# Performance work log

Hardware: AMD Instinct MI355X
Metric: run time of the kernel (lower is better)

## Reference

```python
import jax, jax.numpy as jnp
import numpy as np

NTOKENS = 8192
TOPK = 2
E = 8
K = 1024  # hidden
N = 1024  # ffn shard (ffn_hidden // ffn_tp)


def setup_inputs() -> dict:
    key = jax.random.key(0)
    k1, k2, k3 = jax.random.split(key, 3)
    x = jax.random.normal(k1, (NTOKENS, K), jnp.float32) * 0.02
    # weights stored [E, N, K] (transpose_weight=True path in the torch module)
    weights = jax.random.normal(k2, (E, N, K), jnp.float32) * 0.02
    # random top-k expert assignment per token, then derive the expert-sorted
    # dispatch permutation (scatter_index) and per-expert counts (splits),
    # exactly the invariants flux.prepare_moe_ag_scatter_args relies on.
    experts = jax.random.randint(k3, (NTOKENS, TOPK), 0, E)
    flat = experts.reshape(-1)                       # [NTOKENS*TOPK]
    order = jnp.argsort(flat, stable=True)           # output row -> flat slot
    m = NTOKENS * TOPK
    pos = jnp.zeros((m,), jnp.int32).at[order].set(jnp.arange(m, dtype=jnp.int32))
    scatter_index = pos.reshape(NTOKENS, TOPK)       # flat slot -> output row
    splits = jnp.bincount(flat, length=E).astype(jnp.int32)
    return {"x": x, "weights": weights, "scatter_index": scatter_index, "splits": splits}


def reference(x, weights, scatter_index, splits):
    """MoE AG-scatter grouped GEMM (single-rank semantics: all-gather = identity).

    For each output row s (rows sorted by expert): out[s] = x[token(s)] @ W[e(s)].T
    where token(s) = gather_A_index[s] // topk and e(s) comes from splits.
    """
    ntokens, topk = scatter_index.shape
    e, n, k = weights.shape
    m_out = ntokens * topk  # total dispatched rows
    # inverse permutation: output row s -> flattened (token, slot) index
    gather_a = jnp.argsort(scatter_index.reshape(-1), stable=True)  # [m_out]
    token_of_row = gather_a // topk                                  # [m_out]
    expert_of_row = jnp.repeat(jnp.arange(e, dtype=jnp.int32), splits,
                               total_repeat_length=m_out)            # [m_out]
    # compute each token against every expert once (E/topk redundancy), then
    # gather the (token, expert) pairs -- avoids per-row weight materialization
    y_all = jnp.einsum('tk,enk->ten', x, weights)   # [ntokens, E, N]
    out = y_all[token_of_row, expert_of_row]        # [m_out, N]
    return out
```

## Files before the change

### kernel.cpp

```cpp
#include <hip/hip_runtime.h>
#include <hip/hip_bf16.h>

#define NTOK   8192
#define TOPK   2
#define NEXP   8
#define KDIM   1024
#define NDIM   1024
#define MOUT   (NTOK * TOPK)
#define BM     128
#define BN     128
#define BK     64
#define MAXT   (MOUT / BM + NEXP)
#define ROWTOK 1024

#define XB_OFF   (128 * 1024)
#define XB_BYTES (NTOK * KDIM * 2)
#define WB_OFF   (XB_OFF + XB_BYTES)
#define WB_BYTES (NEXP * NDIM * KDIM * 2)
#define WS_NEED  ((size_t)(WB_OFF + WB_BYTES))

typedef unsigned short ushort_t;
typedef __attribute__((ext_vector_type(8))) short short8;
typedef __attribute__((ext_vector_type(4))) float floatx4;
typedef __attribute__((address_space(1))) const unsigned int gu32;
typedef __attribute__((address_space(3))) unsigned int lu32;

__global__ void moe_setup(const int* __restrict__ scatter,
                          const int* __restrict__ splits,
                          int* __restrict__ ws) {
  int tid = blockIdx.x * blockDim.x + threadIdx.x;
  if (tid < MOUT) {
    int s = scatter[tid];
    ws[ROWTOK + s] = tid / TOPK;
  }
  if (tid == 0) {
    int nt = 0, off = 0;
    for (int e = 0; e < NEXP; ++e) {
      int end = off + splits[e];
      for (int r0 = off; r0 < end; r0 += BM) {
        ws[16 + 3 * nt + 0] = r0;
        ws[16 + 3 * nt + 1] = (end - r0 < BM) ? (end - r0) : BM;
        ws[16 + 3 * nt + 2] = e;
        ++nt;
      }
      off = end;
    }
    ws[0] = nt;
    for (int t = nt; t < MAXT; ++t) {
      ws[16 + 3 * t + 0] = 0;
      ws[16 + 3 * t + 1] = 0;
      ws[16 + 3 * t + 2] = 0;
    }
  }
}

__global__ __launch_bounds__(256)
void convert_both(const float* __restrict__ x, const float* __restrict__ w,
                  ushort_t* __restrict__ xb, ushort_t* __restrict__ wb) {
  const int N4X = NTOK * KDIM / 4;
  const int N4W = NEXP * NDIM * KDIM / 4;
  int idx = blockIdx.x * 256 + threadIdx.x;
  for (int i = idx; i < N4X + N4W; i += gridDim.x * 256) {
    float4 v = (i < N4X) ? ((const float4*)x)[i] : ((const float4*)w)[i - N4X];
    union { __hip_bfloat162 h; unsigned int u; } lo, hi;
    lo.h = __float22bfloat162_rn(make_float2(v.x, v.y));
    hi.h = __float22bfloat162_rn(make_float2(v.z, v.w));
    uint2 u2; u2.x = lo.u; u2.y = hi.u;
    if (i < N4X) ((uint2*)xb)[i] = u2;
    else         ((uint2*)wb)[i - N4X] = u2;
  }
}

__global__ __launch_bounds__(256, 3)
void moe_gemm_fast(const ushort_t* __restrict__ xb,
                   const ushort_t* __restrict__ wbm,
                   const int* __restrict__ ws,
                   float* __restrict__ out) {
  __shared__ ushort_t As[BM * BK];
  __shared__ ushort_t Bs[BN * BK];

  const int slot = blockIdx.x;
  const int rows = ws[16 + 3 * slot + 1];
  if (rows == 0) return;
  const int row0 = ws[16 + 3 * slot + 0];
  const int e    = ws[16 + 3 * slot + 2];
  const int c0   = blockIdx.y * BN;

  const int tid  = threadIdx.x;
  const int lane = tid & 63;
  const int wave = tid >> 6;
  const int wm   = (wave >> 1) * 64;
  const int wn   = (wave & 1) * 64;
  const int quad = lane >> 4;
  const int l16  = lane & 15;

  const int* __restrict__ row_token = ws + ROWTOK;

  const int lrow8  = lane >> 3;
  const int gchunk = (lane & 7) ^ lrow8;

  const ushort_t* aptr[4];
  const ushort_t* bptr[4];
#pragma unroll
  for (int t = 0; t < 4; ++t) {
    int r  = wave * 32 + t * 8 + lrow8;
    int rc = (r < rows) ? r : (rows - 1);
    aptr[t] = xb + (size_t)row_token[row0 + rc] * KDIM + gchunk * 8;
    bptr[t] = wbm + ((size_t)e * NDIM + c0 + r) * KDIM + gchunk * 8;
  }

  floatx4 zero = {0.f, 0.f, 0.f, 0.f};
  floatx4 acc[4][4];
#pragma unroll
  for (int i = 0; i < 4; ++i)
#pragma unroll
    for (int j = 0; j < 4; ++j) acc[i][j] = zero;

#pragma unroll 4
  for (int kk = 0; kk < KDIM; kk += BK) {
#pragma unroll
    for (int t = 0; t < 4; ++t) {
      __builtin_amdgcn_global_load_lds(
          (gu32*)(const void*)(aptr[t] + kk),
          (lu32*)(void*)(As + (wave * 32 + t * 8) * BK), 16, 0, 0);
      __builtin_amdgcn_global_load_lds(
          (gu32*)(const void*)(bptr[t] + kk),
          (lu32*)(void*)(Bs + (wave * 32 + t * 8) * BK), 16, 0, 0);
    }
    __syncthreads();

#pragma unroll
    for (int k2 = 0; k2 < 2; ++k2) {
      short8 af[4], bf[4];
#pragma unroll
      for (int i = 0; i < 4; ++i) {
        int m = wm + i * 16 + l16;
        af[i] = *(const short8*)(&As[m * BK + (((k2 * 4 + quad) ^ (m & 7)) * 8)]);
      }
#pragma unroll
      for (int j = 0; j < 4; ++j) {
        int n = wn + j * 16 + l16;
        bf[j] = *(const short8*)(&Bs[n * BK + (((k2 * 4 + quad) ^ (n & 7)) * 8)]);
      }
#pragma unroll
      for (int i = 0; i < 4; ++i)
#pragma unroll
        for (int j = 0; j < 4; ++j)
          acc[i][j] = __builtin_amdgcn_mfma_f32_16x16x32_bf16(af[i], bf[j],
                                                              acc[i][j], 0, 0, 0);
    }
    __syncthreads();
  }

#pragma unroll
  for (int i = 0; i < 4; ++i) {
#pragma unroll
    for (int r = 0; r < 4; ++r) {
      int lrow = wm + i * 16 + quad * 4 + r;
      if (lrow < rows) {
        float* o = out + (size_t)(row0 + lrow) * NDIM + c0 + wn + l16;
#pragma unroll
        for (int j = 0; j < 4; ++j) o[j * 16] = acc[i][j][r];
      }
    }
  }
}

__global__ __launch_bounds__(256)
void moe_gemm_fallback(const float* __restrict__ x,
                       const float* __restrict__ w,
                       const int* __restrict__ ws,
                       float* __restrict__ out) {
  __shared__ ushort_t As[BM * BK];
  __shared__ ushort_t Bs[BN * BK];

  const int slot = blockIdx.x;
  const int rows = ws[16 + 3 * slot + 1];
  if (rows == 0) return;
  const int row0 = ws[16 + 3 * slot + 0];
  const int e    = ws[16 + 3 * slot + 2];
  const int c0   = blockIdx.y * BN;

  const int tid  = threadIdx.x;
  const int lane = tid & 63;
  const int wave = tid >> 6;
  const int wm   = (wave >> 1) * 64;
  const int wn   = (wave & 1) * 64;
  const int quad = lane >> 4;
  const int l16  = lane & 15;

  const int* __restrict__ row_token = ws + ROWTOK;

  const int f4    = tid & 15;
  const int rbase = tid >> 4;
  const int swz   = (f4 >> 1) ^ (rbase & 7);
  const int wroff = rbase * BK + swz * 8 + (f4 & 1) * 4;

  const float* __restrict__ wb = w + ((size_t)e * NDIM + c0) * KDIM;
  const float* pA[8];
#pragma unroll
  for (int i = 0; i < 8; ++i) {
    int r = rbase + i * 16;
    pA[i] = (r < rows) ? (x + (size_t)row_token[row0 + r] * KDIM + f4 * 4)
                       : nullptr;
  }
  const float* pB0 = wb + (size_t)rbase * KDIM + f4 * 4;

  floatx4 zero = {0.f, 0.f, 0.f, 0.f};
  floatx4 acc[4][4];
#pragma unroll
  for (int i = 0; i < 4; ++i)
#pragma unroll
    for (int j = 0; j < 4; ++j) acc[i][j] = zero;

#pragma unroll 1
  for (int kk = 0; kk < KDIM; kk += BK) {
#pragma unroll
    for (int i = 0; i < 8; ++i) {
      float4 v = {0.f, 0.f, 0.f, 0.f};
      if (pA[i]) v = *(const float4*)(pA[i] + kk);
      union { __hip_bfloat162 h; unsigned int u; } lo, hi;
      lo.h = __float22bfloat162_rn(make_float2(v.x, v.y));
      hi.h = __float22bfloat162_rn(make_float2(v.z, v.w));
      uint2 u2; u2.x = lo.u; u2.y = hi.u;
      *(uint2*)(&As[wroff + i * 16 * BK]) = u2;
    }
#pragma unroll
    for (int i = 0; i < 8; ++i) {
      float4 v = *(const float4*)(pB0 + (size_t)i * 16 * KDIM + kk);
      union { __hip_bfloat162 h; unsigned int u; } lo, hi;
      lo.h = __float22bfloat162_rn(make_float2(v.x, v.y));
      hi.h = __float22bfloat162_rn(make_float2(v.z, v.w));
      uint2 u2; u2.x = lo.u; u2.y = hi.u;
      *(uint2*)(&Bs[wroff + i * 16 * BK]) = u2;
    }
    __syncthreads();
#pragma unroll
    for (int k2 = 0; k2 < 2; ++k2) {
      short8 af[4], bf[4];
#pragma unroll
      for (int i = 0; i < 4; ++i) {
        int m = wm + i * 16 + l16;
        af[i] = *(const short8*)(&As[m * BK + ((k2 * 4 + quad) ^ (m & 7)) * 8]);
      }
#pragma unroll
      for (int j = 0; j < 4; ++j) {
        int n = wn + j * 16 + l16;
        bf[j] = *(const short8*)(&Bs[n * BK + ((k2 * 4 + quad) ^ (n & 7)) * 8]);
      }
#pragma unroll
      for (int i = 0; i < 4; ++i)
#pragma unroll
        for (int j = 0; j < 4; ++j)
          acc[i][j] = __builtin_amdgcn_mfma_f32_16x16x32_bf16(af[i], bf[j],
                                                              acc[i][j], 0, 0, 0);
    }
    __syncthreads();
  }

#pragma unroll
  for (int i = 0; i < 4; ++i) {
#pragma unroll
    for (int r = 0; r < 4; ++r) {
      int lrow = wm + i * 16 + quad * 4 + r;
      if (lrow < rows) {
        float* o = out + (size_t)(row0 + lrow) * NDIM + c0 + wn + l16;
#pragma unroll
        for (int j = 0; j < 4; ++j) o[j * 16] = acc[i][j][r];
      }
    }
  }
}

extern "C" void kernel_launch(void* const* d_in, const int* in_sizes, int n_in,
                              void* d_out, int out_size, void* d_ws, size_t ws_size,
                              hipStream_t stream) {
  const float* x       = (const float*)d_in[0];
  const float* weights = (const float*)d_in[1];
  const int*   scatter = (const int*)d_in[2];
  const int*   splits  = (const int*)d_in[3];
  float*       out     = (float*)d_out;
  int*         ws      = (int*)d_ws;

  moe_setup<<<dim3(MOUT / 256), dim3(256), 0, stream>>>(scatter, splits, ws);

  if (ws_size >= WS_NEED) {
    ushort_t* xb = (ushort_t*)((char*)d_ws + XB_OFF);
    ushort_t* wb = (ushort_t*)((char*)d_ws + WB_OFF);
    convert_both<<<dim3(2048), dim3(256), 0, stream>>>(x, weights, xb, wb);
    moe_gemm_fast<<<dim3(MAXT, NDIM / BN), dim3(256), 0, stream>>>(xb, wb, ws, out);
  } else {
    moe_gemm_fallback<<<dim3(MAXT, NDIM / BN), dim3(256), 0, stream>>>(x, weights,
                                                                       ws, out);
  }
}
```

Measured before the change: 168.4 us.

## Fuse setup into convert kernel and remap GEMM tiles for expert-interleaved scheduling

Removes the separate setup launch by folding the row-token map and tile-table construction into the bf16 conversion kernel. The GEMM grid becomes a flat 1D list of tiles read from a precomputed table. The table interleaves experts across consecutive block IDs (slot p = count*8 + expert), presumably so blocks running at the same time, and likely the per-XCD round-robin placement, share an expert's weights in cache. The cost is a serial single-thread table build of about 1100 entries inside one thread of the conversion kernel, which may delay that block.

```diff
diff --git a/kernel.cpp b/kernel.cpp
--- a/kernel.cpp
+++ b/kernel.cpp
@@ -11,8 +11,12 @@
 #define BN     128
 #define BK     64
 #define MAXT   (MOUT / BM + NEXP)
-#define ROWTOK 1024
-
+#define NBLK   (MAXT * (NDIM / BN))
+#define CLSCAP (NBLK / 8)
+
+#define TBL      64
+#define SPILL    8192
+#define ROWTOK   16384
 #define XB_OFF   (128 * 1024)
 #define XB_BYTES (NTOK * KDIM * 2)
 #define WB_OFF   (XB_OFF + XB_BYTES)
@@ -25,42 +29,58 @@
 typedef __attribute__((address_space(1))) const unsigned int gu32;
 typedef __attribute__((address_space(3))) unsigned int lu32;
 
-__global__ void moe_setup(const int* __restrict__ scatter,
-                          const int* __restrict__ splits,
-                          int* __restrict__ ws) {
-  int tid = blockIdx.x * blockDim.x + threadIdx.x;
-  if (tid < MOUT) {
-    int s = scatter[tid];
-    ws[ROWTOK + s] = tid / TOPK;
-  }
-  if (tid == 0) {
-    int nt = 0, off = 0;
-    for (int e = 0; e < NEXP; ++e) {
-      int end = off + splits[e];
-      for (int r0 = off; r0 < end; r0 += BM) {
-        ws[16 + 3 * nt + 0] = r0;
-        ws[16 + 3 * nt + 1] = (end - r0 < BM) ? (end - r0) : BM;
-        ws[16 + 3 * nt + 2] = e;
-        ++nt;
-      }
-      off = end;
-    }
-    ws[0] = nt;
-    for (int t = nt; t < MAXT; ++t) {
-      ws[16 + 3 * t + 0] = 0;
-      ws[16 + 3 * t + 1] = 0;
-      ws[16 + 3 * t + 2] = 0;
-    }
+__device__ void build_table(const int* __restrict__ splits, int* __restrict__ ws) {
+  for (int p = 0; p < NBLK; ++p) ws[TBL + 4 * p + 1] = 0;
+  int cnt[8];
+#pragma unroll
+  for (int e = 0; e < 8; ++e) cnt[e] = 0;
+  int nspill = 0;
+  int off = 0;
+  for (int e = 0; e < NEXP; ++e) {
+    int end = off + splits[e];
+    for (int r0 = off; r0 < end; r0 += BM) {
+      int rows = end - r0; if (rows > BM) rows = BM;
+      for (int cy = 0; cy < NDIM / BN; ++cy) {
+        if (cnt[e] < CLSCAP) {
+          int p = (cnt[e]++) * 8 + e;
+          ws[TBL + 4 * p + 0] = r0;  ws[TBL + 4 * p + 1] = rows;
+          ws[TBL + 4 * p + 2] = e;   ws[TBL + 4 * p + 3] = cy;
+        } else {
+          ws[SPILL + 4 * nspill + 0] = r0;  ws[SPILL + 4 * nspill + 1] = rows;
+          ws[SPILL + 4 * nspill + 2] = e;   ws[SPILL + 4 * nspill + 3] = cy;
+          ++nspill;
+        }
+      }
+    }
+    off = end;
+  }
+  int e2 = 0;
+  for (int s = 0; s < nspill; ++s) {
+    while (cnt[e2] >= CLSCAP) ++e2;
+    int p = (cnt[e2]++) * 8 + e2;
+    ws[TBL + 4 * p + 0] = ws[SPILL + 4 * s + 0];
+    ws[TBL + 4 * p + 1] = ws[SPILL + 4 * s + 1];
+    ws[TBL + 4 * p + 2] = ws[SPILL + 4 * s + 2];
+    ws[TBL + 4 * p + 3] = ws[SPILL + 4 * s + 3];
   }
 }
 
 __global__ __launch_bounds__(256)
-void convert_both(const float* __restrict__ x, const float* __restrict__ w,
-                  ushort_t* __restrict__ xb, ushort_t* __restrict__ wb) {
+void convert_setup(const float* __restrict__ x, const float* __restrict__ w,
+                   const int* __restrict__ scatter, const int* __restrict__ splits,
+                   ushort_t* __restrict__ xb, ushort_t* __restrict__ wb,
+                   int* __restrict__ ws) {
   const int N4X = NTOK * KDIM / 4;
   const int N4W = NEXP * NDIM * KDIM / 4;
-  int idx = blockIdx.x * 256 + threadIdx.x;
-  for (int i = idx; i < N4X + N4W; i += gridDim.x * 256) {
+  int gtid = blockIdx.x * 256 + threadIdx.x;
+
+  if (gtid < MOUT) {
+    int s = scatter[gtid];
+    ws[ROWTOK + s] = gtid / TOPK;
+  }
+  if (gtid == 0) build_table(splits, ws);
+
+  for (int i = gtid; i < N4X + N4W; i += gridDim.x * 256) {
     float4 v = (i < N4X) ? ((const float4*)x)[i] : ((const float4*)w)[i - N4X];
     union { __hip_bfloat162 h; unsigned int u; } lo, hi;
     lo.h = __float22bfloat162_rn(make_float2(v.x, v.y));
@@ -79,12 +99,12 @@
   __shared__ ushort_t As[BM * BK];
   __shared__ ushort_t Bs[BN * BK];
 
-  const int slot = blockIdx.x;
-  const int rows = ws[16 + 3 * slot + 1];
+  int4 ent = ((const int4*)(ws + TBL))[blockIdx.x];
+  const int rows = ent.y;
   if (rows == 0) return;
-  const int row0 = ws[16 + 3 * slot + 0];
-  const int e    = ws[16 + 3 * slot + 2];
-  const int c0   = blockIdx.y * BN;
+  const int row0 = ent.x;
+  const int e    = ent.z;
+  const int c0   = ent.w * BN;
 
   const int tid  = threadIdx.x;
   const int lane = tid & 63;
@@ -166,6 +186,17 @@
   }
 }
 
+__global__ void setup_only(const int* __restrict__ scatter,
+                           const int* __restrict__ splits,
+                           int* __restrict__ ws) {
+  int gtid = blockIdx.x * blockDim.x + threadIdx.x;
+  if (gtid < MOUT) {
+    int s = scatter[gtid];
+    ws[ROWTOK + s] = gtid / TOPK;
+  }
+  if (gtid == 0) build_table(splits, ws);
+}
+
 __global__ __launch_bounds__(256)
 void moe_gemm_fallback(const float* __restrict__ x,
                        const float* __restrict__ w,
@@ -174,12 +205,12 @@
   __shared__ ushort_t As[BM * BK];
   __shared__ ushort_t Bs[BN * BK];
 
-  const int slot = blockIdx.x;
-  const int rows = ws[16 + 3 * slot + 1];
+  int4 ent = ((const int4*)(ws + TBL))[blockIdx.x];
+  const int rows = ent.y;
   if (rows == 0) return;
-  const int row0 = ws[16 + 3 * slot + 0];
-  const int e    = ws[16 + 3 * slot + 2];
-  const int c0   = blockIdx.y * BN;
+  const int row0 = ent.x;
+  const int e    = ent.z;
+  const int c0   = ent.w * BN;
 
   const int tid  = threadIdx.x;
   const int lane = tid & 63;
@@ -282,15 +313,14 @@
   float*       out     = (float*)d_out;
   int*         ws      = (int*)d_ws;
 
-  moe_setup<<<dim3(MOUT / 256), dim3(256), 0, stream>>>(scatter, splits, ws);
-
   if (ws_size >= WS_NEED) {
     ushort_t* xb = (ushort_t*)((char*)d_ws + XB_OFF);
     ushort_t* wb = (ushort_t*)((char*)d_ws + WB_OFF);
-    convert_both<<<dim3(2048), dim3(256), 0, stream>>>(x, weights, xb, wb);
-    moe_gemm_fast<<<dim3(MAXT, NDIM / BN), dim3(256), 0, stream>>>(xb, wb, ws, out);
+    convert_setup<<<dim3(2048), dim3(256), 0, stream>>>(x, weights, scatter,
+                                                        splits, xb, wb, ws);
+    moe_gemm_fast<<<dim3(NBLK), dim3(256), 0, stream>>>(xb, wb, ws, out);
   } else {
-    moe_gemm_fallback<<<dim3(MAXT, NDIM / BN), dim3(256), 0, stream>>>(x, weights,
-                                                                       ws, out);
-  }
-}
+    setup_only<<<dim3(MOUT / 256), dim3(256), 0, stream>>>(scatter, splits, ws);
+    moe_gemm_fallback<<<dim3(NBLK), dim3(256), 0, stream>>>(x, weights, ws, out);
+  }
+}
```

Measured after the change: 249.6 us. +48.2%, slower.
